# Performance work log

Hardware: AMD Instinct MI355X
Metric: run time of the kernel (lower is better)

## Reference

```python
import jax, jax.numpy as jnp
import numpy as np

MODEL_DIM = 512
NUM_HEADS = 8
HEAD_DIM = MODEL_DIM // NUM_HEADS  # 64
NUM_NODE = 1024
CLUSTER = 128
S = 60
EMBED = 0.5


def setup_inputs() -> dict:
    key = jax.random.key(0)
    ks = jax.random.split(key, 16)
    d = MODEL_DIM
    sc = 1.0 / np.sqrt(d)
    inp = {
        "x": jax.random.normal(ks[0], (4, 12, NUM_NODE, d), dtype=jnp.float32),
        "Wq": jax.random.normal(ks[1], (d, d), dtype=jnp.float32) * sc,
        "bq": jnp.zeros((d,), jnp.float32),
        "Wk": jax.random.normal(ks[2], (d, d), dtype=jnp.float32) * sc,
        "bk": jnp.zeros((d,), jnp.float32),
        "Wv": jax.random.normal(ks[3], (d, d), dtype=jnp.float32) * sc,
        "bv": jnp.zeros((d,), jnp.float32),
        "We": jax.random.normal(ks[4], (d, d), dtype=jnp.float32) * sc,
        "be": jnp.zeros((d,), jnp.float32),
        "Wo": jax.random.normal(ks[5], (d, d), dtype=jnp.float32) * sc,
        "bo": jnp.zeros((d,), jnp.float32),
        # adp_pos is initialized to zeros in torch; use small randn for a non-degenerate test
        "adp_pos": jax.random.normal(ks[6], (NUM_NODE, CLUSTER), dtype=jnp.float32) * 0.02,
        "U1": jax.random.normal(ks[7], (HEAD_DIM, S), dtype=jnp.float32) * np.sqrt(2.0 / (HEAD_DIM + S)),
        "U2": jax.random.normal(ks[8], (S, HEAD_DIM), dtype=jnp.float32) * np.sqrt(2.0 / (S + HEAD_DIM)),
    }
    return inp


def _split_heads(t):
    # torch.cat(torch.split(t, head_dim, -1), 0): heads stacked head-major on batch dim
    return jnp.concatenate(jnp.split(t, NUM_HEADS, axis=-1), axis=0)


def _merge_heads(t):
    return jnp.concatenate(jnp.split(t, NUM_HEADS, axis=0), axis=-1)


def _pool_nodes(t):
    # AdaptiveAvgPool2d((CLUSTER, None)) on (B,T,N,D) with N % CLUSTER == 0 -> block mean
    B, T, N, D = t.shape
    return t.reshape(B, T, CLUSTER, N // CLUSTER, D).mean(axis=3)


def reference(x, Wq, bq, Wk, bk, Wv, bv, We, be, Wo, bo, adp_pos, U1, U2):
    q = x @ Wq.T + bq                      # (B,T,N,D)
    k = _pool_nodes(x @ Wk.T + bk)          # (B,T,C,D)
    v = _pool_nodes(x @ Wv.T + bv)          # (B,T,C,D)
    ev = x @ We.T + be                      # (B,T,N,D)

    qh = _split_heads(q)                    # (B*H,T,N,d)
    kh = _split_heads(k)                    # (B*H,T,C,d)
    vh = _split_heads(v)                    # (B*H,T,C,d)
    evh = _split_heads(ev)                  # (B*H,T,N,d)

    # external attention branch: softmax over node dim (-2)
    exa = jax.nn.softmax(evh @ U1, axis=-2)  # (B*H,T,N,S)
    exa_val = (exa @ U2) * EMBED + evh       # (B*H,T,N,d)

    score = jnp.einsum("btnd,btcd->btnc", qh, kh) / np.sqrt(HEAD_DIM)
    score = score + adp_pos[None, None]      # (B*H,T,N,C)
    attn = jax.nn.softmax(score, axis=-1)

    out = attn @ vh + exa_val                # (B*H,T,N,d)
    out = _merge_heads(out)                  # (B,T,N,D)
    return out @ Wo.T + bo
```

## Files before the change

### kernel.cpp

```cpp
#include <hip/hip_runtime.h>


#define LOG2E 1.44269504088896f

typedef __attribute__((ext_vector_type(4))) float f32x4;
typedef __attribute__((ext_vector_type(8))) short bf16x8;

__device__ __forceinline__ unsigned short f2bf(float f) {
    union { float f; unsigned u; } v; v.f = f;
    unsigned r = (v.u + 0x7fffu + ((v.u >> 16) & 1u)) >> 16;
    return (unsigned short)r;
}
__device__ __forceinline__ float bf2f(unsigned short h) {
    union { unsigned u; float f; } v; v.u = ((unsigned)h) << 16;
    return v.f;
}
__device__ __forceinline__ unsigned cvt_pk_bf16(float lo, float hi) {
    unsigned r;
    asm("v_cvt_pk_bf16_f32 %0, %1, %2" : "=v"(r) : "v"(lo), "v"(hi));
    return r;
}
__device__ __forceinline__ void gll16(const void* g, void* l) {
    __builtin_amdgcn_global_load_lds((const __attribute__((address_space(1))) void*)g,
                                     (__attribute__((address_space(3))) void*)l,
                                     16, 0, 0);
}

__global__ void cvt_w(const float* __restrict__ Wq, const float* __restrict__ Wk,
                      const float* __restrict__ Wv, const float* __restrict__ We,
                      const float* __restrict__ Wo, const float* __restrict__ U1,
                      const float* __restrict__ U2,
                      const float* __restrict__ bq, const float* __restrict__ bk,
                      const float* __restrict__ bv, const float* __restrict__ be,
                      unsigned short* __restrict__ Wqe, unsigned short* __restrict__ Wkv,
                      unsigned short* __restrict__ Wob, unsigned short* __restrict__ U1T,
                      unsigned short* __restrict__ U2bT,
                      float* __restrict__ bqe, float* __restrict__ bkv)
{
    int i = blockIdx.x * 256 + threadIdx.x;
    if (i < 524288) {
        int r = i >> 9;
        float v = (r < 512) ? Wq[i] * 0.125f : We[i - 262144];
        Wqe[i] = f2bf(v);
    } else if (i < 1048576) {
        int j = i - 524288; int r = j >> 9;
        float v = (r < 512) ? Wk[j] : Wv[j - 262144];
        Wkv[j] = f2bf(v);
    } else if (i < 1310720) {
        int j = i - 1048576;
        Wob[j] = f2bf(Wo[j]);
    } else if (i < 1314816) {
        int j = i - 1310720; int s = j >> 6, k = j & 63;
        U1T[j] = (s < 60) ? f2bf(U1[k * 60 + s]) : (unsigned short)0;
    } else if (i < 1318912) {
        int j = i - 1314816; int d = j >> 6, s = j & 63;
        U2bT[j] = (s < 60) ? f2bf(U2[s * 64 + d] * 0.5f) : (unsigned short)0;
    } else if (i < 1319936) {
        int j = i - 1318912;
        bqe[j] = (j < 512) ? bq[j] * 0.125f : be[j - 512];
    } else if (i < 1320960) {
        int j = i - 1319936;
        bkv[j] = (j < 512) ? bk[j] : bv[j - 512];
    }
}

__global__ void cvt_pool(const float* __restrict__ x, unsigned short* __restrict__ xb,
                         unsigned short* __restrict__ xpb)
{
    int i = blockIdx.x * 256 + threadIdx.x;
    int d4 = i & 127;
    int btc = i >> 7;
    int bt = btc >> 7, c = btc & 127;
    long base = ((long)(bt * 1024 + c * 8)) * 128 + d4;
    const float4* src = (const float4*)x + base;
    ushort4* dst = (ushort4*)xb + base;
    float sx = 0.f, sy = 0.f, sz = 0.f, sw = 0.f;
#pragma unroll
    for (int j = 0; j < 8; j++) {
        float4 v = src[(long)j * 128];
        sx += v.x; sy += v.y; sz += v.z; sw += v.w;
        ushort4 o;
        o.x = f2bf(v.x); o.y = f2bf(v.y); o.z = f2bf(v.z); o.w = f2bf(v.w);
        dst[(long)j * 128] = o;
    }
    ushort4 p;
    p.x = f2bf(sx * 0.125f); p.y = f2bf(sy * 0.125f);
    p.z = f2bf(sz * 0.125f); p.w = f2bf(sw * 0.125f);
    ((ushort4*)xpb)[(long)btc * 128 + d4] = p;
}

template <int OUTF32>
__global__ __launch_bounds__(256, 4) void gemm_bt(
    const unsigned short* __restrict__ A, const unsigned short* __restrict__ W,
    const float* __restrict__ bias, void* __restrict__ Cout,
    int M, int N, int K)
{
    __shared__ __attribute__((aligned(16))) unsigned short As[128 * 32];
    __shared__ __attribute__((aligned(16))) unsigned short Bs[128 * 32];
    const int tid = threadIdx.x;
    const int wave = tid >> 6, lane = tid & 63;
    const int quad = lane >> 4, l16 = lane & 15;
    const int m0 = blockIdx.x * 128, n0 = blockIdx.y * 128;
    const int wm = (wave & 1) * 64, wn = (wave >> 1) * 64;

    f32x4 acc[4][4];
#pragma unroll
    for (int i = 0; i < 4; i++)
#pragma unroll
        for (int j = 0; j < 4; j++) acc[i][j] = (f32x4){0.f, 0.f, 0.f, 0.f};

    const int c0 = tid, c1 = tid + 256;
    const int r0 = c0 >> 2, kc0 = (c0 & 3) * 8;
    const int r1 = c1 >> 2, kc1 = (c1 & 3) * 8;
    const unsigned short* pa0 = A + (long)(m0 + r0) * K + kc0;
    const unsigned short* pa1 = A + (long)(m0 + r1) * K + kc1;
    const unsigned short* pb0 = W + (long)(n0 + r0) * K + kc0;
    const unsigned short* pb1 = W + (long)(n0 + r1) * K + kc1;
    unsigned short* lA0 = &As[wave * 512];
    unsigned short* lA1 = &As[2048 + wave * 512];
    unsigned short* lB0 = &Bs[wave * 512];
    unsigned short* lB1 = &Bs[2048 + wave * 512];

    for (int k0 = 0; k0 < K; k0 += 32) {
        gll16(pa0 + k0, lA0);
        gll16(pa1 + k0, lA1);
        gll16(pb0 + k0, lB0);
        gll16(pb1 + k0, lB1);
        __syncthreads();
        bf16x8 af[4], bfr[4];
#pragma unroll
        for (int t = 0; t < 4; t++)
            af[t] = *(const bf16x8*)&As[(wm + t * 16 + l16) * 32 + quad * 8];
#pragma unroll
        for (int t = 0; t < 4; t++)
            bfr[t] = *(const bf16x8*)&Bs[(wn + t * 16 + l16) * 32 + quad * 8];
#pragma unroll
        for (int tm = 0; tm < 4; tm++)
#pragma unroll
            for (int tn = 0; tn < 4; tn++)
                acc[tm][tn] = __builtin_amdgcn_mfma_f32_16x16x32_bf16(
                    af[tm], bfr[tn], acc[tm][tn], 0, 0, 0);
        __syncthreads();
    }

#pragma unroll
    for (int tm = 0; tm < 4; tm++)
#pragma unroll
        for (int tn = 0; tn < 4; tn++) {
            int cc = n0 + wn + tn * 16 + l16;
            float bv = bias[cc];
#pragma unroll
            for (int r = 0; r < 4; r++) {
                int rr = m0 + wm + tm * 16 + quad * 4 + r;
                float v = acc[tm][tn][r] + bv;
                if (OUTF32) ((float*)Cout)[(long)rr * N + cc] = v;
                else        ((unsigned short*)Cout)[(long)rr * N + cc] = f2bf(v);
            }
        }
}

__global__ __launch_bounds__(256, 4) void g2_kv(
    const unsigned short* __restrict__ A, const unsigned short* __restrict__ W,
    const float* __restrict__ bias, unsigned short* __restrict__ kvK,
    unsigned short* __restrict__ vT)
{
    const int K = 512;
    __shared__ __attribute__((aligned(16))) unsigned short As[128 * 32];
    __shared__ __attribute__((aligned(16))) unsigned short Bs[128 * 32];
    const int tid = threadIdx.x;
    const int wave = tid >> 6, lane = tid & 63;
    const int quad = lane >> 4, l16 = lane & 15;
    const int m0 = blockIdx.x * 128, n0 = blockIdx.y * 128;
    const int wm = (wave & 1) * 64, wn = (wave >> 1) * 64;

    f32x4 acc[4][4];
#pragma unroll
    for (int i = 0; i < 4; i++)
#pragma unroll
        for (int j = 0; j < 4; j++) acc[i][j] = (f32x4){0.f, 0.f, 0.f, 0.f};

    const int c0 = tid, c1 = tid + 256;
    const int r0 = c0 >> 2, kc0 = (c0 & 3) * 8;
    const int r1 = c1 >> 2, kc1 = (c1 & 3) * 8;
    const unsigned short* pa0 = A + (long)(m0 + r0) * K + kc0;
    const unsigned short* pa1 = A + (long)(m0 + r1) * K + kc1;
    const unsigned short* pb0 = W + (long)(n0 + r0) * K + kc0;
    const unsigned short* pb1 = W + (long)(n0 + r1) * K + kc1;
    unsigned short* lA0 = &As[wave * 512];
    unsigned short* lA1 = &As[2048 + wave * 512];
    unsigned short* lB0 = &Bs[wave * 512];
    unsigned short* lB1 = &Bs[2048 + wave * 512];

    for (int k0 = 0; k0 < K; k0 += 32) {
        gll16(pa0 + k0, lA0);
        gll16(pa1 + k0, lA1);
        gll16(pb0 + k0, lB0);
        gll16(pb1 + k0, lB1);
        __syncthreads();
        bf16x8 af[4], bfr[4];
#pragma unroll
        for (int t = 0; t < 4; t++)
            af[t] = *(const bf16x8*)&As[(wm + t * 16 + l16) * 32 + quad * 8];
#pragma unroll
        for (int t = 0; t < 4; t++)
            bfr[t] = *(const bf16x8*)&Bs[(wn + t * 16 + l16) * 32 + quad * 8];
#pragma unroll
        for (int tm = 0; tm < 4; tm++)
#pragma unroll
            for (int tn = 0; tn < 4; tn++)
                acc[tm][tn] = __builtin_amdgcn_mfma_f32_16x16x32_bf16(
                    af[tm], bfr[tn], acc[tm][tn], 0, 0, 0);
        __syncthreads();
    }

#pragma unroll
    for (int tm = 0; tm < 4; tm++)
#pragma unroll
        for (int tn = 0; tn < 4; tn++) {
            int cc = n0 + wn + tn * 16 + l16;
            float bv = bias[cc];
            int rrb = m0 + wm + tm * 16 + quad * 4;
            if (cc < 512) {
#pragma unroll
                for (int r = 0; r < 4; r++)
                    kvK[(long)(rrb + r) * 512 + cc] = f2bf(acc[tm][tn][r] + bv);
            } else {
                int hh = (cc - 512) >> 6, dd = (cc - 512) & 63;
                int btv = rrb >> 7, cv = rrb & 127;
                ushort4 o;
                o.x = f2bf(acc[tm][tn][0] + bv);
                o.y = f2bf(acc[tm][tn][1] + bv);
                o.z = f2bf(acc[tm][tn][2] + bv);
                o.w = f2bf(acc[tm][tn][3] + bv);
                *(ushort4*)(vT + ((long)(btv * 8 + hh) * 64 + dd) * 128 + cv) = o;
            }
        }
}

__global__ __launch_bounds__(256, 2) void ez_kernel(
    const unsigned short* __restrict__ qev, const unsigned short* __restrict__ U1T,
    unsigned short* __restrict__ Z)
{
    __shared__ __attribute__((aligned(16))) unsigned short evs[128 * 72];
    __shared__ __attribute__((aligned(16))) unsigned short u1s[64 * 72];
    int tid = threadIdx.x, bx = blockIdx.x;
    int bt = bx >> 6, h = (bx >> 3) & 7, nb = bx & 7;
    int wave = tid >> 6, lane = tid & 63, quad = lane >> 4, l16 = lane & 15;

#pragma unroll
    for (int i = 0; i < 4; i++) {
        int c = tid + i * 256; int row = c >> 3, kc = (c & 7) * 8;
        *(int4*)&evs[row * 72 + kc] =
            *(const int4*)(qev + ((long)(bt * 1024 + nb * 128 + row)) * 1024 + 512 + h * 64 + kc);
    }
#pragma unroll
    for (int i = 0; i < 2; i++) {
        int c = tid + i * 256; int row = c >> 3, kc = (c & 7) * 8;
        *(int4*)&u1s[row * 72 + kc] = *(const int4*)(U1T + row * 64 + kc);
    }
    __syncthreads();

    f32x4 acc[2][4];
#pragma unroll
    for (int i = 0; i < 2; i++)
#pragma unroll
        for (int t = 0; t < 4; t++) acc[i][t] = (f32x4){0.f, 0.f, 0.f, 0.f};

#pragma unroll
    for (int kt = 0; kt < 2; kt++) {
        bf16x8 a[2], b[4];
#pragma unroll
        for (int i = 0; i < 2; i++)
            a[i] = *(const bf16x8*)&evs[((wave * 2 + i) * 16 + l16) * 72 + kt * 32 + quad * 8];
#pragma unroll
        for (int t = 0; t < 4; t++)
            b[t] = *(const bf16x8*)&u1s[(t * 16 + l16) * 72 + kt * 32 + quad * 8];
#pragma unroll
        for (int i = 0; i < 2; i++)
#pragma unroll
            for (int t = 0; t < 4; t++)
                acc[i][t] = __builtin_amdgcn_mfma_f32_16x16x32_bf16(a[i], b[t], acc[i][t], 0, 0, 0);
    }

    long zb = (long)(bt * 8 + h) * 1024 + nb * 128;
#pragma unroll
    for (int i = 0; i < 2; i++)
#pragma unroll
        for (int t = 0; t < 4; t++) {
            int s = t * 16 + l16;
            if (s < 60) {
#pragma unroll
                for (int r = 0; r < 4; r++) {
                    int rr = (wave * 2 + i) * 16 + quad * 4 + r;
                    Z[(zb + rr) * 60 + s] = f2bf(acc[i][t][r]);
                }
            }
        }
}

__global__ __launch_bounds__(1024, 4) void es_kernel(
    const unsigned short* __restrict__ Z, float* __restrict__ mS, float* __restrict__ lSinv)
{
    __shared__ float ms[16][64];
    __shared__ float ls[16][64];
    int tid = threadIdx.x;
    int s = tid & 63, g = tid >> 6;
    long zb = (long)blockIdx.x * 1024 * 60;
    float m = -1e30f, l = 0.f;
    if (s < 60) {
        for (int r = 0; r < 64; r++) {
            float z = bf2f(Z[zb + (long)(g * 64 + r) * 60 + s]);
            float nm = fmaxf(m, z);
            l = l * exp2f((m - nm) * LOG2E) + exp2f((z - nm) * LOG2E);
            m = nm;
        }
    }
    ms[g][s] = m; ls[g][s] = l;
    __syncthreads();
    if (tid < 60) {
        float M = ms[0][tid];
#pragma unroll
        for (int gg = 1; gg < 16; gg++) M = fmaxf(M, ms[gg][tid]);
        float L = 0.f;
#pragma unroll
        for (int gg = 0; gg < 16; gg++) L += ls[gg][tid] * exp2f((ms[gg][tid] - M) * LOG2E);
        mS[blockIdx.x * 60 + tid] = M;
        lSinv[blockIdx.x * 60 + tid] = 1.0f / L;
    }
}

__global__ __launch_bounds__(256, 4) void att_kernel(
    const unsigned short* __restrict__ qev, const unsigned short* __restrict__ kvK,
    const unsigned short* __restrict__ vT, const unsigned short* __restrict__ Z,
    const float* __restrict__ mS, const float* __restrict__ lI,
    const float* __restrict__ adp, const unsigned short* __restrict__ U2bT,
    unsigned short* __restrict__ attn_out)
{
    __shared__ __attribute__((aligned(16))) unsigned short Ps[128 * 136];

    int tid = threadIdx.x, bx = blockIdx.x;
    int bt = bx >> 6, h = (bx >> 3) & 7, nb = bx & 7;
    int wave = tid >> 6, lane = tid & 63, quad = lane >> 4, l16 = lane & 15;
    int n0 = nb * 128;
    const int g = bt * 8 + h;
    const long qrow0 = (long)bt * 1024 + n0;

    f32x4 sc[2][8];
#pragma unroll
    for (int i = 0; i < 2; i++)
#pragma unroll
        for (int t = 0; t < 8; t++) sc[i][t] = (f32x4){0.f, 0.f, 0.f, 0.f};

#pragma unroll
    for (int kt = 0; kt < 2; kt++) {
        bf16x8 qf[2];
#pragma unroll
        for (int i = 0; i < 2; i++)
            qf[i] = *(const bf16x8*)(qev + (qrow0 + wave * 32 + i * 16 + l16) * 1024
                                     + h * 64 + kt * 32 + quad * 8);
#pragma unroll
        for (int tn = 0; tn < 8; tn++) {
            bf16x8 kf = *(const bf16x8*)(kvK + (long)(bt * 128 + tn * 16 + l16) * 512
                                         + h * 64 + kt * 32 + quad * 8);
#pragma unroll
            for (int i = 0; i < 2; i++)
                sc[i][tn] = __builtin_amdgcn_mfma_f32_16x16x32_bf16(kf, qf[i], sc[i][tn], 0, 0, 0);
        }
    }

#pragma unroll
    for (int i = 0; i < 2; i++) {
        const int qr = wave * 32 + i * 16 + l16;
        float m = -1e30f;
#pragma unroll
        for (int tn = 0; tn < 8; tn++) {
            float4 ad = *(const float4*)(adp + (long)(n0 + qr) * 128 + tn * 16 + quad * 4);
            sc[i][tn][0] += ad.x; sc[i][tn][1] += ad.y;
            sc[i][tn][2] += ad.z; sc[i][tn][3] += ad.w;
#pragma unroll
            for (int r = 0; r < 4; r++) m = fmaxf(m, sc[i][tn][r]);
        }
        m = fmaxf(m, __shfl_xor(m, 16, 64));
        m = fmaxf(m, __shfl_xor(m, 32, 64));
        float s = 0.f;
#pragma unroll
        for (int tn = 0; tn < 8; tn++)
#pragma unroll
            for (int r = 0; r < 4; r++) {
                float p = exp2f((sc[i][tn][r] - m) * LOG2E);
                sc[i][tn][r] = p; s += p;
            }
        s += __shfl_xor(s, 16, 64);
        s += __shfl_xor(s, 32, 64);
        float rinv = 1.0f / s;
#pragma unroll
        for (int tn = 0; tn < 8; tn++) {
            uint2 w2;
            w2.x = cvt_pk_bf16(sc[i][tn][0] * rinv, sc[i][tn][1] * rinv);
            w2.y = cvt_pk_bf16(sc[i][tn][2] * rinv, sc[i][tn][3] * rinv);
            *(uint2*)&Ps[qr * 136 + tn * 16 + quad * 4] = w2;
        }
    }

    f32x4 oc[2][4];
#pragma unroll
    for (int i = 0; i < 2; i++)
#pragma unroll
        for (int t = 0; t < 4; t++) oc[i][t] = (f32x4){0.f, 0.f, 0.f, 0.f};

#pragma unroll
    for (int kt = 0; kt < 4; kt++) {
        bf16x8 a[2];
#pragma unroll
        for (int i = 0; i < 2; i++)
            a[i] = *(const bf16x8*)&Ps[((wave * 2 + i) * 16 + l16) * 136 + kt * 32 + quad * 8];
#pragma unroll
        for (int tn = 0; tn < 4; tn++) {
            bf16x8 b = *(const bf16x8*)(vT + ((long)g * 64 + tn * 16 + l16) * 128
                                        + kt * 32 + quad * 8);
#pragma unroll
            for (int i = 0; i < 2; i++)
                oc[i][tn] = __builtin_amdgcn_mfma_f32_16x16x32_bf16(a[i], b, oc[i][tn], 0, 0, 0);
        }
    }

#pragma unroll
    for (int kt = 0; kt < 2; kt++) {
        int sb = kt * 32 + quad * 8;
        float4 ma = *(const float4*)(mS + (long)g * 60 + sb);
        float4 mb2 = *(const float4*)(mS + (long)g * 60 + sb + 4);
        float4 la = *(const float4*)(lI + (long)g * 60 + sb);
        float4 lb2 = *(const float4*)(lI + (long)g * 60 + sb + 4);
        float mv[8] = {ma.x, ma.y, ma.z, ma.w, mb2.x, mb2.y, mb2.z, mb2.w};
        float lv[8] = {la.x, la.y, la.z, la.w, lb2.x, lb2.y, lb2.z, lb2.w};
        bf16x8 ea[2];
#pragma unroll
        for (int i = 0; i < 2; i++) {
            int row = (wave * 2 + i) * 16 + l16;
            const unsigned short* zp = Z + ((long)g * 1024 + n0 + row) * 60 + sb;
            uint2 z0 = *(const uint2*)zp;
            uint2 z1 = *(const uint2*)(zp + 4);
            unsigned zz[4] = {z0.x, z0.y, z1.x, z1.y};
            unsigned short es_[8];
#pragma unroll
            for (int j = 0; j < 8; j++) {
                unsigned short zh = (unsigned short)((zz[j >> 1] >> ((j & 1) * 16)) & 0xffff);
                float e = (sb + j < 60)
                    ? exp2f((bf2f(zh) - mv[j]) * LOG2E) * lv[j] : 0.f;
                es_[j] = f2bf(e);
            }
            ea[i] = *(bf16x8*)es_;
        }
#pragma unroll
        for (int tn = 0; tn < 4; tn++) {
            bf16x8 b = *(const bf16x8*)(U2bT + (tn * 16 + l16) * 64 + sb);
#pragma unroll
            for (int i = 0; i < 2; i++)
                oc[i][tn] = __builtin_amdgcn_mfma_f32_16x16x32_bf16(ea[i], b, oc[i][tn], 0, 0, 0);
        }
    }

#pragma unroll
    for (int i = 0; i < 2; i++)
#pragma unroll
        for (int tn = 0; tn < 4; tn++)
#pragma unroll
            for (int r = 0; r < 4; r++) {
                int rr = (wave * 2 + i) * 16 + quad * 4 + r;
                int cc = tn * 16 + l16;
                float ev = bf2f(qev[(qrow0 + rr) * 1024 + 512 + h * 64 + cc]);
                attn_out[(qrow0 + rr) * 512 + h * 64 + cc] = f2bf(oc[i][tn][r] + ev);
            }
}

extern "C" void kernel_launch(void* const* d_in, const int* in_sizes, int n_in,
                              void* d_out, int out_size, void* d_ws, size_t ws_size,
                              hipStream_t stream)
{
    const float* x   = (const float*)d_in[0];
    const float* Wq  = (const float*)d_in[1];
    const float* bq  = (const float*)d_in[2];
    const float* Wk  = (const float*)d_in[3];
    const float* bk  = (const float*)d_in[4];
    const float* Wv  = (const float*)d_in[5];
    const float* bv  = (const float*)d_in[6];
    const float* We  = (const float*)d_in[7];
    const float* be  = (const float*)d_in[8];
    const float* Wo  = (const float*)d_in[9];
    const float* bo  = (const float*)d_in[10];
    const float* adp = (const float*)d_in[11];
    const float* U1  = (const float*)d_in[12];
    const float* U2  = (const float*)d_in[13];

    char* ws = (char*)d_ws;
    unsigned short* xb   = (unsigned short*)(ws + 0);
    unsigned short* aout = xb;
    unsigned short* xpb  = (unsigned short*)(ws + 50331648);
    unsigned short* qev  = (unsigned short*)(ws + 56623104);
    unsigned short* kvK  = (unsigned short*)(ws + 157286400);
    unsigned short* vT   = (unsigned short*)(ws + 163577856);
    unsigned short* Zb   = (unsigned short*)(ws + 169869312);
    unsigned short* Wqe  = (unsigned short*)(ws + 217055232);
    unsigned short* Wkv  = (unsigned short*)(ws + 218103808);
    unsigned short* Wob  = (unsigned short*)(ws + 219152384);
    unsigned short* U1T  = (unsigned short*)(ws + 219676672);
    unsigned short* U2bT = (unsigned short*)(ws + 219684864);
    float*          mSb  = (float*)(ws + 219693056);
    float*          lIb  = (float*)(ws + 219785216);
    float*          bqe  = (float*)(ws + 219877376);
    float*          bkv  = (float*)(ws + 219881472);

    cvt_w<<<5160, 256, 0, stream>>>(Wq, Wk, Wv, We, Wo, U1, U2, bq, bk, bv, be,
                                    Wqe, Wkv, Wob, U1T, U2bT, bqe, bkv);
    cvt_pool<<<3072, 256, 0, stream>>>(x, xb, xpb);

    gemm_bt<0><<<dim3(384, 8), 256, 0, stream>>>(xb,  Wqe, bqe, (void*)qev, 49152, 1024, 512);
    g2_kv<<<dim3(48, 8), 256, 0, stream>>>(xpb, Wkv, bkv, kvK, vT);

    ez_kernel<<<3072, 256, 0, stream>>>(qev, U1T, Zb);
    es_kernel<<<384, 1024, 0, stream>>>(Zb, mSb, lIb);
    att_kernel<<<3072, 256, 0, stream>>>(qev, kvK, vT, Zb, mSb, lIb, adp, U2bT, aout);

    gemm_bt<1><<<dim3(384, 4), 256, 0, stream>>>(aout, Wob, bo, d_out, 49152, 512, 512);
}
```

Baseline: 473.9 us.

## Write Q and EV in head-major layout and swizzle attention P tile

Adds a dedicated Q/EV projection GEMM whose epilogue writes q and ev into separate head-major (bt,h,n,d) buffers, so the ez and attention kernels read contiguous 64-wide rows instead of strided 1024-wide rows. The attention kernel's P shared-memory tile drops padding in favour of an XOR swizzle, which shrinks LDS, and launch bounds are raised to allow five blocks per CU. The GEMM epilogue now does scattered 2-byte stores with a stride of 64 elements, which may cost more than the previous row-major writes.

```diff
diff --git a/kernel.cpp b/kernel.cpp
--- a/kernel.cpp
+++ b/kernel.cpp
@@ -89,6 +89,77 @@
     ((ushort4*)xpb)[(long)btc * 128 + d4] = p;
 }
 
+__global__ __launch_bounds__(256, 4) void g1_qev(
+    const unsigned short* __restrict__ A, const unsigned short* __restrict__ W,
+    const float* __restrict__ bias, unsigned short* __restrict__ qh,
+    unsigned short* __restrict__ evh)
+{
+    const int K = 512;
+    __shared__ __attribute__((aligned(16))) unsigned short As[128 * 32];
+    __shared__ __attribute__((aligned(16))) unsigned short Bs[128 * 32];
+    const int tid = threadIdx.x;
+    const int wave = tid >> 6, lane = tid & 63;
+    const int quad = lane >> 4, l16 = lane & 15;
+    const int m0 = blockIdx.x * 128, n0 = blockIdx.y * 128;
+    const int wm = (wave & 1) * 64, wn = (wave >> 1) * 64;
+
+    f32x4 acc[4][4];
+#pragma unroll
+    for (int i = 0; i < 4; i++)
+#pragma unroll
+        for (int j = 0; j < 4; j++) acc[i][j] = (f32x4){0.f, 0.f, 0.f, 0.f};
+
+    const int c0 = tid, c1 = tid + 256;
+    const int r0 = c0 >> 2, kc0 = (c0 & 3) * 8;
+    const int r1 = c1 >> 2, kc1 = (c1 & 3) * 8;
+    const unsigned short* pa0 = A + (long)(m0 + r0) * K + kc0;
+    const unsigned short* pa1 = A + (long)(m0 + r1) * K + kc1;
+    const unsigned short* pb0 = W + (long)(n0 + r0) * K + kc0;
+    const unsigned short* pb1 = W + (long)(n0 + r1) * K + kc1;
+    unsigned short* lA0 = &As[wave * 512];
+    unsigned short* lA1 = &As[2048 + wave * 512];
+    unsigned short* lB0 = &Bs[wave * 512];
+    unsigned short* lB1 = &Bs[2048 + wave * 512];
+
+    for (int k0 = 0; k0 < K; k0 += 32) {
+        gll16(pa0 + k0, lA0);
+        gll16(pa1 + k0, lA1);
+        gll16(pb0 + k0, lB0);
+        gll16(pb1 + k0, lB1);
+        __syncthreads();
+        bf16x8 af[4], bfr[4];
+#pragma unroll
+        for (int t = 0; t < 4; t++)
+            af[t] = *(const bf16x8*)&As[(wm + t * 16 + l16) * 32 + quad * 8];
+#pragma unroll
+        for (int t = 0; t < 4; t++)
+            bfr[t] = *(const bf16x8*)&Bs[(wn + t * 16 + l16) * 32 + quad * 8];
+#pragma unroll
+        for (int tm = 0; tm < 4; tm++)
+#pragma unroll
+            for (int tn = 0; tn < 4; tn++)
+                acc[tm][tn] = __builtin_amdgcn_mfma_f32_16x16x32_bf16(
+                    af[tm], bfr[tn], acc[tm][tn], 0, 0, 0);
+        __syncthreads();
+    }
+
+#pragma unroll
+    for (int tm = 0; tm < 4; tm++)
+#pragma unroll
+        for (int tn = 0; tn < 4; tn++) {
+            int cc = n0 + wn + tn * 16 + l16;
+            float bv = bias[cc];
+            int hq = (cc >> 6) & 7, dd = cc & 63;
+            int rr0 = m0 + wm + tm * 16 + quad * 4;
+            int bt = rr0 >> 10, n = rr0 & 1023;
+            unsigned short* dst = ((cc < 512) ? qh : evh)
+                + ((long)(bt * 8 + hq) * 1024 + n) * 64 + dd;
+#pragma unroll
+            for (int r = 0; r < 4; r++)
+                dst[(long)r * 64] = f2bf(acc[tm][tn][r] + bv);
+        }
+}
+
 template <int OUTF32>
 __global__ __launch_bounds__(256, 4) void gemm_bt(
     const unsigned short* __restrict__ A, const unsigned short* __restrict__ W,
@@ -238,7 +309,7 @@
 }
 
 __global__ __launch_bounds__(256, 2) void ez_kernel(
-    const unsigned short* __restrict__ qev, const unsigned short* __restrict__ U1T,
+    const unsigned short* __restrict__ evh, const unsigned short* __restrict__ U1T,
     unsigned short* __restrict__ Z)
 {
     __shared__ __attribute__((aligned(16))) unsigned short evs[128 * 72];
@@ -246,12 +317,12 @@
     int tid = threadIdx.x, bx = blockIdx.x;
     int bt = bx >> 6, h = (bx >> 3) & 7, nb = bx & 7;
     int wave = tid >> 6, lane = tid & 63, quad = lane >> 4, l16 = lane & 15;
+    long gb = ((long)(bt * 8 + h) * 1024 + nb * 128) * 64;
 
 #pragma unroll
     for (int i = 0; i < 4; i++) {
         int c = tid + i * 256; int row = c >> 3, kc = (c & 7) * 8;
-        *(int4*)&evs[row * 72 + kc] =
-            *(const int4*)(qev + ((long)(bt * 1024 + nb * 128 + row)) * 1024 + 512 + h * 64 + kc);
+        *(int4*)&evs[row * 72 + kc] = *(const int4*)(evh + gb + row * 64 + kc);
     }
 #pragma unroll
     for (int i = 0; i < 2; i++) {
@@ -329,21 +400,22 @@
     }
 }
 
-__global__ __launch_bounds__(256, 4) void att_kernel(
-    const unsigned short* __restrict__ qev, const unsigned short* __restrict__ kvK,
-    const unsigned short* __restrict__ vT, const unsigned short* __restrict__ Z,
+__global__ __launch_bounds__(256, 5) void att_kernel(
+    const unsigned short* __restrict__ qh, const unsigned short* __restrict__ evh,
+    const unsigned short* __restrict__ kvK, const unsigned short* __restrict__ vT,
+    const unsigned short* __restrict__ Z,
     const float* __restrict__ mS, const float* __restrict__ lI,
     const float* __restrict__ adp, const unsigned short* __restrict__ U2bT,
     unsigned short* __restrict__ attn_out)
 {
-    __shared__ __attribute__((aligned(16))) unsigned short Ps[128 * 136];
+    __shared__ __attribute__((aligned(16))) unsigned short Ps[128 * 128];
 
     int tid = threadIdx.x, bx = blockIdx.x;
     int bt = bx >> 6, h = (bx >> 3) & 7, nb = bx & 7;
     int wave = tid >> 6, lane = tid & 63, quad = lane >> 4, l16 = lane & 15;
     int n0 = nb * 128;
     const int g = bt * 8 + h;
-    const long qrow0 = (long)bt * 1024 + n0;
+    const long grow0 = (long)g * 1024 + n0;
 
     f32x4 sc[2][8];
 #pragma unroll
@@ -356,8 +428,8 @@
         bf16x8 qf[2];
 #pragma unroll
         for (int i = 0; i < 2; i++)
-            qf[i] = *(const bf16x8*)(qev + (qrow0 + wave * 32 + i * 16 + l16) * 1024
-                                     + h * 64 + kt * 32 + quad * 8);
+            qf[i] = *(const bf16x8*)(qh + (grow0 + wave * 32 + i * 16 + l16) * 64
+                                     + kt * 32 + quad * 8);
 #pragma unroll
         for (int tn = 0; tn < 8; tn++) {
             bf16x8 kf = *(const bf16x8*)(kvK + (long)(bt * 128 + tn * 16 + l16) * 512
@@ -398,7 +470,8 @@
             uint2 w2;
             w2.x = cvt_pk_bf16(sc[i][tn][0] * rinv, sc[i][tn][1] * rinv);
             w2.y = cvt_pk_bf16(sc[i][tn][2] * rinv, sc[i][tn][3] * rinv);
-            *(uint2*)&Ps[qr * 136 + tn * 16 + quad * 4] = w2;
+            unsigned wb = (unsigned)(qr * 256 + tn * 32 + quad * 8) ^ ((unsigned)(qr & 7) << 4);
+            *(uint2*)((char*)Ps + wb) = w2;
         }
     }
 
@@ -412,8 +485,11 @@
     for (int kt = 0; kt < 4; kt++) {
         bf16x8 a[2];
 #pragma unroll
-        for (int i = 0; i < 2; i++)
-            a[i] = *(const bf16x8*)&Ps[((wave * 2 + i) * 16 + l16) * 136 + kt * 32 + quad * 8];
+        for (int i = 0; i < 2; i++) {
+            int row = wave * 32 + i * 16 + l16;
+            unsigned rb = (unsigned)(row * 256 + kt * 64 + quad * 16) ^ ((unsigned)(row & 7) << 4);
+            a[i] = *(const bf16x8*)((char*)Ps + rb);
+        }
 #pragma unroll
         for (int tn = 0; tn < 4; tn++) {
             bf16x8 b = *(const bf16x8*)(vT + ((long)g * 64 + tn * 16 + l16) * 128
@@ -468,8 +544,9 @@
             for (int r = 0; r < 4; r++) {
                 int rr = (wave * 2 + i) * 16 + quad * 4 + r;
                 int cc = tn * 16 + l16;
-                float ev = bf2f(qev[(qrow0 + rr) * 1024 + 512 + h * 64 + cc]);
-                attn_out[(qrow0 + rr) * 512 + h * 64 + cc] = f2bf(oc[i][tn][r] + ev);
+                float ev = bf2f(evh[(grow0 + rr) * 64 + cc]);
+                attn_out[((long)bt * 1024 + n0 + rr) * 512 + h * 64 + cc]
+                    = f2bf(oc[i][tn][r] + ev);
             }
 }
 
@@ -496,7 +573,8 @@
     unsigned short* xb   = (unsigned short*)(ws + 0);
     unsigned short* aout = xb;
     unsigned short* xpb  = (unsigned short*)(ws + 50331648);
-    unsigned short* qev  = (unsigned short*)(ws + 56623104);
+    unsigned short* qh   = (unsigned short*)(ws + 56623104);
+    unsigned short* evh  = (unsigned short*)(ws + 106954752);
     unsigned short* kvK  = (unsigned short*)(ws + 157286400);
     unsigned short* vT   = (unsigned short*)(ws + 163577856);
     unsigned short* Zb   = (unsigned short*)(ws + 169869312);
@@ -514,12 +592,12 @@
                                     Wqe, Wkv, Wob, U1T, U2bT, bqe, bkv);
     cvt_pool<<<3072, 256, 0, stream>>>(x, xb, xpb);
 
-    gemm_bt<0><<<dim3(384, 8), 256, 0, stream>>>(xb,  Wqe, bqe, (void*)qev, 49152, 1024, 512);
+    g1_qev<<<dim3(384, 8), 256, 0, stream>>>(xb, Wqe, bqe, qh, evh);
     g2_kv<<<dim3(48, 8), 256, 0, stream>>>(xpb, Wkv, bkv, kvK, vT);
 
-    ez_kernel<<<3072, 256, 0, stream>>>(qev, U1T, Zb);
+    ez_kernel<<<3072, 256, 0, stream>>>(evh, U1T, Zb);
     es_kernel<<<384, 1024, 0, stream>>>(Zb, mSb, lIb);
-    att_kernel<<<3072, 256, 0, stream>>>(qev, kvK, vT, Zb, mSb, lIb, adp, U2bT, aout);
+    att_kernel<<<3072, 256, 0, stream>>>(qh, evh, kvK, vT, Zb, mSb, lIb, adp, U2bT, aout);
 
     gemm_bt<1><<<dim3(384, 4), 256, 0, stream>>>(aout, Wob, bo, d_out, 49152, 512, 512);
 }
```

After: 479.3 us. About the same (+1.2%).
